# Optimization experiments

Measured on AMD Instinct MI355X. Metric: run time of the kernel, lower is better.

Reference implementation:

```python
import jax, jax.numpy as jnp
import numpy as np

B, S, H, J, LAT, OBS = 256, 128, 1024, 12, 64, 51
NL = 13                  # fk_model link count
PD = (NL + 1) * 3        # pos_dim = 42
FPS = 30.0
ACT_SCALE = 0.25
SMIN, SMAX = 0.05, 0.5
PIN = 2 * J + OBS + LAT  # 139


def setup_inputs() -> dict:
    key = jax.random.key(0)
    ks = jax.random.split(key, 16)
    rn = lambda k, shape, s=0.02: jax.random.normal(k, shape, dtype=jnp.float32) * s
    return dict(
        z=jax.random.normal(ks[0], (B, LAT), jnp.float32),
        obs_seq=jax.random.normal(ks[1], (B, S, OBS), jnp.float32),
        W1=rn(ks[2], (H, PIN)), b1=jnp.zeros((H,), jnp.float32),
        g1=jnp.ones((H,), jnp.float32), be1=jnp.zeros((H,), jnp.float32),
        W2=rn(ks[3], (H, H)), b2=jnp.zeros((H,), jnp.float32),
        g2=jnp.ones((H,), jnp.float32), be2=jnp.zeros((H,), jnp.float32),
        Wa1=rn(ks[4], (H, H)), ba1=jnp.zeros((H,), jnp.float32),
        Wa2=rn(ks[5], (J, H)), ba2=jnp.zeros((J,), jnp.float32),
        Wo=rn(ks[6], (3, H)), bo=jnp.zeros((3,), jnp.float32),
        Wv=rn(ks[7], (PD, H)), bv=jnp.full((PD,), -2.0, jnp.float32),  # torch init: zeros weight, bias=-2 (we keep small random W for non-degenerate grads)
        alpha_logits=jnp.full((J,), float(np.log(0.3)), jnp.float32),
        fk_W=rn(ks[8], (NL * 3, J), 0.1), fk_b=rn(ks[9], (NL * 3,), 0.1),  # linear FK surrogate
        pos_mean=rn(ks[10], (NL + 1, 3), 0.1),
        pos_std=1.0 + jax.random.uniform(ks[11], (NL + 1, 3), jnp.float32),
        joint_lower=jnp.full((J,), -2.0, jnp.float32),
        joint_upper=jnp.full((J,), 2.0, jnp.float32),
        default_dof_pos=rn(ks[12], (J,), 0.3),
    )


def _layernorm(x, g, b):
    m = jnp.mean(x, axis=-1, keepdims=True)
    v = jnp.var(x, axis=-1, keepdims=True)
    return (x - m) * jax.lax.rsqrt(v + 1e-5) * g + b


def reference(z, obs_seq, W1, b1, g1, be1, W2, b2, g2, be2, Wa1, ba1, Wa2, ba2,
              Wo, bo, Wv, bv, alpha_logits, fk_W, fk_b, pos_mean, pos_std,
              joint_lower, joint_upper, default_dof_pos):
    j_range = (joint_upper - joint_lower) / 2.0
    j_mean = (joint_upper + joint_lower) / 2.0
    alpha = jax.nn.sigmoid(alpha_logits)
    Bsz = z.shape[0]

    def step(carry, obs_t):
        pj, pdq = carry                                 # [B,J] each
        jn = (pj - j_mean) / j_range
        x = jnp.concatenate([jn, pdq, obs_t, z], axis=-1)   # [B,PIN]
        h = jax.nn.relu(_layernorm(x @ W1.T + b1, g1, be1))
        h = jax.nn.relu(_layernorm(h @ W2.T + b2, g2, be2))  # [B,H]
        a = jnp.tanh(jax.nn.relu(h @ Wa1.T + ba1) @ Wa2.T + ba2)  # [B,J]
        tgt = a * ACT_SCALE + default_dof_pos
        cj = jnp.clip(pj + alpha * (tgt - pj), joint_lower, joint_upper)
        obj = h @ Wo.T + bo                             # [B,3]
        # torch detaches the carried state (prev_joints/prev_dq)
        cdq = (cj - pj) * FPS
        new_carry = (jax.lax.stop_gradient(cj), jax.lax.stop_gradient(cdq))
        return new_carry, (h, a, cj, obj)

    pj0 = jnp.broadcast_to(default_dof_pos, (Bsz, J))
    pdq0 = jnp.zeros((Bsz, J), z.dtype)
    _, (hs, acts, joints, objs) = jax.lax.scan(step, (pj0, pdq0), jnp.swapaxes(obs_seq, 0, 1))

    features_seq = jnp.swapaxes(hs, 0, 1)    # [B,S,H]
    actions_seq = jnp.swapaxes(acts, 0, 1)   # [B,S,J]
    joint_traj = jnp.swapaxes(joints, 0, 1)  # [B,S,J]
    object_traj = jnp.swapaxes(objs, 0, 1)   # [B,S,3]

    agent_traj = joint_traj @ fk_W.T + fk_b  # [B,S,NL*3] linear FK surrogate
    combined = jnp.concatenate([agent_traj, object_traj], axis=-1)
    combined = combined.reshape(Bsz, S, NL + 1, 3)
    graph_x_mu = ((combined - pos_mean) / pos_std).reshape(Bsz, S, -1)  # [B,S,PD]

    sigma = SMIN + (SMAX - SMIN) * jax.nn.sigmoid(features_seq @ Wv.T + bv)
    log_sigma_pos = jnp.log(sigma)           # [B,S,PD]
    return (graph_x_mu, joint_traj, actions_seq, log_sigma_pos)
```

## Files before the change

kernel.cpp:

```cpp
#include <hip/hip_runtime.h>
#include <math.h>


#define NB 256
#define NS 128
#define NH 1024
#define NJ 12
#define NPIN 139
#define NPD 42
#define WPG 32
#define BROW 32
#define W2S 1032
#define AS 1032
#define SLOTSTRIDE 1024

typedef __attribute__((ext_vector_type(8))) short short8;
typedef __attribute__((ext_vector_type(4))) float f32x4;
typedef __attribute__((ext_vector_type(4))) unsigned short u16x4;

struct Params {
  const float* z; const float* obs; const float* W1; const float* b1;
  const float* g1; const float* be1; const float* W2; const float* b2;
  const float* g2; const float* be2; const float* Wa1; const float* ba1;
  const float* Wa2; const float* ba2; const float* Wo; const float* bo;
  const float* Wv; const float* bv; const float* alog; const float* fkW;
  const float* fkb; const float* pmean; const float* pstd; const float* jlo;
  const float* jhi; const float* ddp;
  float* out_gmu; float* out_joint; float* out_act; float* out_ls;
  float* zc; float* pa; float* part1; float* part2;
  unsigned short* y1b; unsigned short* y2b;
  unsigned short* wa1b; unsigned short* wexb;
  unsigned int* gcnt; unsigned int* slots;
};

__device__ __forceinline__ unsigned short f2bf(float x) {
  union { float f; unsigned u; } v; v.f = x;
  unsigned r = v.u + 0x7FFFu + ((v.u >> 16) & 1u);
  return (unsigned short)(r >> 16);
}
__device__ __forceinline__ float bf2f(unsigned short x) {
  union { unsigned u; float f; } v; v.u = ((unsigned)x) << 16;
  return v.f;
}
__device__ __forceinline__ unsigned cvt_pk_bf16(float lo, float hi) {
  unsigned r;
  asm("v_cvt_pk_bf16_f32 %0, %1, %2" : "=v"(r) : "v"(lo), "v"(hi));
  return r;
}
__device__ __forceinline__ void ld16_sc0(const unsigned short* p, short8& d) {
  asm volatile("global_load_dwordx4 %0, %1, off sc0" : "=v"(d) : "v"(p));
}
__device__ __forceinline__ void ldf4_sc0(const float* p, f32x4& d) {
  asm volatile("global_load_dwordx4 %0, %1, off sc0" : "=v"(d) : "v"(p));
}
__device__ __forceinline__ void vwait0() {
  asm volatile("s_waitcnt vmcnt(0)" ::: "memory");
  __builtin_amdgcn_sched_barrier(0);
}

__device__ __forceinline__ f32x4 dot1024(const unsigned short* a, const unsigned short* b) {
  const short8* ap = (const short8*)a;
  const short8* bp = (const short8*)b;
  f32x4 acc0 = {0.f, 0.f, 0.f, 0.f};
  f32x4 acc1 = {0.f, 0.f, 0.f, 0.f};
#pragma unroll 4
  for (int k8 = 0; k8 < 128; k8 += 8) {
    acc0 = __builtin_amdgcn_mfma_f32_16x16x32_bf16(ap[k8], bp[k8], acc0, 0, 0, 0);
    acc1 = __builtin_amdgcn_mfma_f32_16x16x32_bf16(ap[k8 + 4], bp[k8 + 4], acc1, 0, 0, 0);
  }
  return acc0 + acc1;
}

__device__ __forceinline__ void gbar(unsigned int* c, unsigned int target) {
  __threadfence();
  __syncthreads();
  if (threadIdx.x == 0) {
    __hip_atomic_fetch_add(c, 1u, __ATOMIC_RELEASE, __HIP_MEMORY_SCOPE_AGENT);
    unsigned long long t0 = __builtin_amdgcn_s_memrealtime();
    while (__hip_atomic_load(c, __ATOMIC_ACQUIRE, __HIP_MEMORY_SCOPE_AGENT) < target) {
      __builtin_amdgcn_s_sleep(16);
      if (__builtin_amdgcn_s_memrealtime() - t0 > (1ull << 25)) break;
    }
  }
  __syncthreads();
  __threadfence();
}

__device__ __forceinline__ void slot_wait(const unsigned int* sg, unsigned target, int lane) {
  const unsigned int* myslot = sg + (size_t)(lane & 31) * SLOTSTRIDE;
  unsigned long long t0 = __builtin_amdgcn_s_memrealtime();
  for (;;) {
    unsigned v;
    asm volatile("global_load_dword %0, %1, off sc0 sc1\n\t"
                 "s_waitcnt vmcnt(0)"
                 : "=v"(v) : "v"(myslot) : "memory");
    if (__all(v >= target)) break;
    __builtin_amdgcn_s_sleep(1);
    if (__builtin_amdgcn_s_memrealtime() - t0 > (1ull << 23)) break;
  }
}

__device__ __forceinline__ void xbar2(unsigned int* sg, int w, unsigned target,
                                      int wave, int lane) {
  asm volatile("s_waitcnt vmcnt(0)" ::: "memory");
  __syncthreads();
  if (wave == 0) {
    if (lane == 0)
      __hip_atomic_fetch_add(sg + (size_t)w * SLOTSTRIDE, 1u, __ATOMIC_RELAXED,
                             __HIP_MEMORY_SCOPE_AGENT);
    slot_wait(sg, target, lane);
  }
  __syncthreads();
}

__global__ __launch_bounds__(256, 1) void decoder_persistent(Params p) {
  __shared__ unsigned short w2l[BROW * W2S];
  __shared__ unsigned short albuf[BROW * AS];
  __shared__ float g1l[NH], be1l[NH], g2l[NH], be2l[NH];
  __shared__ unsigned short t1l[BROW * 40];
  __shared__ unsigned short wa2l[16 * 40];
  __shared__ float pj_l[BROW * NJ], pdq_l[BROW * NJ];
  __shared__ float alpha_l[NJ], jm_l[NJ], jri_l[NJ], lo_l[NJ], hi_l[NJ], ddp_l[NJ], ba2_l[NJ];
  __shared__ float pm_l[NPD], psi_l[NPD], bv_l[NPD], bo_l[4];

  const int tid = threadIdx.x;
  const int bid = blockIdx.x;
  const int g = bid & 7;
  const int w = bid >> 3;
  const int b0 = g * BROW;
  const int n0 = w * 32;
  const int wave = tid >> 6;
  const int lane = tid & 63;

  unsigned int* sg = p.slots + (size_t)g * WPG * SLOTSTRIDE;
  unsigned short* y1bg = p.y1b + (size_t)g * BROW * NH;
  unsigned short* y2bg = p.y2b + (size_t)g * BROW * NH;
  float* pa_gg = p.pa + (size_t)g * BROW * NJ * 32;
  float* part1g = p.part1 + (size_t)g * BROW * 64;
  float* part2g = p.part2 + (size_t)g * BROW * 128;

  if (tid < NJ) {
    alpha_l[tid] = 1.f / (1.f + expf(-p.alog[tid]));
    float lo = p.jlo[tid], hi = p.jhi[tid];
    jm_l[tid] = 0.5f * (hi + lo);
    jri_l[tid] = 2.f / (hi - lo);
    lo_l[tid] = lo; hi_l[tid] = hi;
    ddp_l[tid] = p.ddp[tid]; ba2_l[tid] = p.ba2[tid];
  }
  if (tid < NPD) { pm_l[tid] = p.pmean[tid]; psi_l[tid] = 1.f / p.pstd[tid]; bv_l[tid] = p.bv[tid]; }
  if (tid < 3) bo_l[tid] = p.bo[tid];
  for (int idx = tid; idx < BROW * NJ; idx += 256) { pj_l[idx] = p.ddp[idx % NJ]; pdq_l[idx] = 0.f; }
  for (int idx = tid; idx < NH; idx += 256) {
    g1l[idx] = p.g1[idx]; be1l[idx] = p.be1[idx];
    g2l[idx] = p.g2[idx]; be2l[idx] = p.be2[idx];
  }
  for (int idx = tid; idx < BROW * NH; idx += 256) {
    int r = idx >> 10, k = idx & (NH - 1);
    w2l[r * W2S + k] = f2bf(p.W2[(size_t)(n0 + r) * NH + k]);
  }
  for (int idx = tid; idx < 16 * 32; idx += 256) {
    int rr = idx >> 5, cc = idx & 31;
    wa2l[rr * 40 + cc] = (rr < NJ) ? f2bf(p.Wa2[(size_t)rr * NH + n0 + cc]) : (unsigned short)0;
  }
  {
    int r = tid >> 3, cq = tid & 7;
    int nb = n0 + cq * 4;
    const float* zr = p.z + (size_t)(b0 + r) * 64;
    const float* w1r = p.W1 + (size_t)nb * NPIN + 75;
    float a0 = p.b1[nb], a1 = p.b1[nb + 1], a2 = p.b1[nb + 2], a3 = p.b1[nb + 3];
    for (int k = 0; k < 64; ++k) {
      float zv = zr[k];
      a0 += zv * w1r[k]; a1 += zv * w1r[NPIN + k];
      a2 += zv * w1r[2 * NPIN + k]; a3 += zv * w1r[3 * NPIN + k];
    }
    f32x4 st = {a0, a1, a2, a3};
    *(f32x4*)(p.zc + (size_t)(b0 + r) * NH + nb) = st;
  }
  for (int idx = tid; idx < 4 * NH; idx += 256) {
    int r = idx >> 10, k = idx & (NH - 1);
    int row = n0 + g * 4 + r;
    p.wa1b[(size_t)row * NH + k] = f2bf(p.Wa1[(size_t)row * NH + k]);
  }
  if (bid == 1) {
    for (int idx = tid; idx < 48 * NH; idx += 256) {
      int r = idx >> 10, k = idx & (NH - 1);
      unsigned short v = 0;
      if (r < 3) v = f2bf(p.Wo[(size_t)r * NH + k]);
      else if (r < 45) v = f2bf(p.Wv[(size_t)(r - 3) * NH + k]);
      p.wexb[idx] = v;
    }
  }
  gbar(p.gcnt, 256u);

  auto stage_ln_apply = [&](const unsigned short* yg, const float* part, bool wide,
                            const float* gl, const float* bl) {
    const int r = tid >> 3, cq = tid & 7;
    const unsigned short* src = yg + (size_t)r * NH + cq * 8;
    unsigned short* dst = &albuf[r * AS + cq * 8];
    short8 v[16];
#pragma unroll
    for (int i = 0; i < 16; ++i) ld16_sc0(src + (size_t)i * 64, v[i]);
    const int fpr = wide ? 128 : 64;
    const float* pp = part + (size_t)r * fpr + cq * (fpr >> 3);
    f32x4 p0, p1, p2 = {0, 0, 0, 0}, p3 = {0, 0, 0, 0};
    ldf4_sc0(pp, p0);
    ldf4_sc0(pp + 4, p1);
    if (wide) { ldf4_sc0(pp + 8, p2); ldf4_sc0(pp + 12, p3); }
    vwait0();
    float s = p0[0] + p0[2] + p1[0] + p1[2];
    float q = p0[1] + p0[3] + p1[1] + p1[3];
    if (wide) {
      s += p2[0] + p2[2] + p3[0] + p3[2];
      q += p2[1] + p2[3] + p3[1] + p3[3];
    }
#pragma unroll
    for (int off = 4; off; off >>= 1) {
      s += __shfl_down(s, off, 8);
      q += __shfl_down(q, off, 8);
    }
    s = __shfl(s, 0, 8); q = __shfl(q, 0, 8);
    float m = s * (1.f / 1024.f);
    float rs = rsqrtf(q * (1.f / 1024.f) - m * m + 1e-5f);
    float nmrs = -m * rs;
#pragma unroll
    for (int i = 0; i < 16; ++i) {
      int c = cq * 8 + i * 64;
      f32x4 ga = *(const f32x4*)(gl + c);
      f32x4 gb = *(const f32x4*)(gl + c + 4);
      f32x4 ba = *(const f32x4*)(bl + c);
      f32x4 bb = *(const f32x4*)(bl + c + 4);
      float xn[8];
#pragma unroll
      for (int jj = 0; jj < 8; ++jj) {
        float x = bf2f((unsigned short)v[i][jj]);
        float tn = fmaf(x, rs, nmrs);
        float gg = (jj < 4) ? ga[jj] : gb[jj - 4];
        float bv2 = (jj < 4) ? ba[jj] : bb[jj - 4];
        xn[jj] = fmaxf(fmaf(tn, gg, bv2), 0.f);
      }
      uint4 pk = {cvt_pk_bf16(xn[0], xn[1]), cvt_pk_bf16(xn[2], xn[3]),
                  cvt_pk_bf16(xn[4], xn[5]), cvt_pk_bf16(xn[6], xn[7])};
      *(uint4*)(dst + i * 64) = pk;
    }
  };

  auto P1_obs = [&](int t) -> f32x4 {
    int r = tid >> 3, cq = tid & 7;
    int nb = n0 + cq * 4;
    f32x4 acc = *(const f32x4*)(p.zc + (size_t)(b0 + r) * NH + nb);
    const float* w1r = p.W1 + (size_t)nb * NPIN;
    const float* ob = p.obs + ((size_t)(b0 + r) * NS + t) * 51;
    for (int o = 0; o < 51; ++o) {
      float ov = ob[o];
      acc[0] += ov * w1r[24 + o]; acc[1] += ov * w1r[NPIN + 24 + o];
      acc[2] += ov * w1r[2 * NPIN + 24 + o]; acc[3] += ov * w1r[3 * NPIN + 24 + o];
    }
    return acc;
  };
  auto P1_fin = [&](f32x4 acc) {
    int r = tid >> 3, cq = tid & 7;
    int nb = n0 + cq * 4;
    float xj[24];
#pragma unroll
    for (int j = 0; j < NJ; ++j) {
      xj[j] = (pj_l[r * NJ + j] - jm_l[j]) * jri_l[j];
      xj[12 + j] = pdq_l[r * NJ + j];
    }
    const float* w1r = p.W1 + (size_t)nb * NPIN;
#pragma unroll
    for (int k = 0; k < 24; ++k) {
      float xv = xj[k];
      acc[0] += xv * w1r[k]; acc[1] += xv * w1r[NPIN + k];
      acc[2] += xv * w1r[2 * NPIN + k]; acc[3] += xv * w1r[3 * NPIN + k];
    }
    u16x4 hv = {f2bf(acc[0]), f2bf(acc[1]), f2bf(acc[2]), f2bf(acc[3])};
    *(u16x4*)(y1bg + (size_t)r * NH + nb) = hv;
    float s = acc[0] + acc[1] + acc[2] + acc[3];
    float q = acc[0] * acc[0] + acc[1] * acc[1] + acc[2] * acc[2] + acc[3] * acc[3];
#pragma unroll
    for (int off = 4; off; off >>= 1) {
      s += __shfl_down(s, off, 8);
      q += __shfl_down(q, off, 8);
    }
    if ((tid & 7) == 0) {
      float* pw = part1g + (size_t)r * 64 + w * 2;
      pw[0] = s; pw[1] = q;
    }
  };

  auto Yphase = [&]() {
    stage_ln_apply(y1bg, part1g, false, g1l, be1l);
    __syncthreads();
    int rt = wave >> 1, ct = wave & 1;
    int kq = (lane >> 4) * 8;
    const unsigned short* a = &albuf[(rt * 16 + (lane & 15)) * AS + kq];
    const unsigned short* b = &w2l[(ct * 16 + (lane & 15)) * W2S + kq];
    f32x4 acc = dot1024(a, b);
    int col = n0 + ct * 16 + (lane & 15);
    float b2v = p.b2[col];
    float sv[4], qv[4];
#pragma unroll
    for (int i = 0; i < 4; ++i) {
      int row = rt * 16 + (lane >> 4) * 4 + i;
      float val = acc[i] + b2v;
      y2bg[(size_t)row * NH + col] = f2bf(val);
      sv[i] = val; qv[i] = val * val;
    }
#pragma unroll
    for (int mask = 1; mask < 16; mask <<= 1) {
#pragma unroll
      for (int i = 0; i < 4; ++i) {
        sv[i] += __shfl_xor(sv[i], mask, 64);
        qv[i] += __shfl_xor(qv[i], mask, 64);
      }
    }
    if ((lane & 15) == 0) {
      int rbase = rt * 16 + (lane >> 4) * 4;
#pragma unroll
      for (int i = 0; i < 4; ++i) {
        float* pw = part2g + (size_t)(rbase + i) * 128 + (w * 2 + ct) * 2;
        pw[0] = sv[i]; pw[1] = qv[i];
      }
    }
  };

  auto Zphase = [&](int t) {
    stage_ln_apply(y2bg, part2g, true, g2l, be2l);
    __syncthreads();
    int rt = wave >> 1, ct = wave & 1;
    int kq = (lane >> 4) * 8;
    {
      const unsigned short* a = &albuf[(rt * 16 + (lane & 15)) * AS + kq];
      const unsigned short* b = p.wa1b + (size_t)(n0 + ct * 16 + (lane & 15)) * NH + kq;
      f32x4 acc = dot1024(a, b);
      int lcol = ct * 16 + (lane & 15);
      float bav = p.ba1[n0 + lcol];
#pragma unroll
      for (int i = 0; i < 4; ++i) {
        int row = rt * 16 + (lane >> 4) * 4 + i;
        t1l[row * 40 + lcol] = f2bf(fmaxf(acc[i] + bav, 0.f));
      }
    }
    __syncthreads();
    if (wave < 2) {
      int k0 = (lane >> 4) * 8;
      short8 a8 = *(const short8*)&t1l[(wave * 16 + (lane & 15)) * 40 + k0];
      short8 b8 = *(const short8*)&wa2l[(lane & 15) * 40 + k0];
      f32x4 z4 = {0.f, 0.f, 0.f, 0.f};
      f32x4 d = __builtin_amdgcn_mfma_f32_16x16x32_bf16(a8, b8, z4, 0, 0, 0);
      int j = lane & 15;
      if (j < NJ) {
#pragma unroll
        for (int i = 0; i < 4; ++i) {
          int row = wave * 16 + (lane >> 4) * 4 + i;
          pa_gg[((size_t)row * NJ + j) * 32 + w] = d[i];
        }
      }
    }
    if (w >= 26 && wave == 3) {
      int e = w - 26, cte = e >> 1, rte = e & 1;
      const unsigned short* a = &albuf[(rte * 16 + (lane & 15)) * AS + kq];
      const unsigned short* b = p.wexb + (size_t)(cte * 16 + (lane & 15)) * NH + kq;
      f32x4 acc = dot1024(a, b);
      int ec = cte * 16 + (lane & 15);
#pragma unroll
      for (int i = 0; i < 4; ++i) {
        int row = rte * 16 + (lane >> 4) * 4 + i;
        int bb = b0 + row;
        if (ec < 3) {
          float val = acc[i] + bo_l[ec];
          p.out_gmu[((size_t)bb * NS + t) * NPD + 39 + ec] = (val - pm_l[39 + ec]) * psi_l[39 + ec];
        } else if (ec < 45) {
          int sv2 = ec - 3;
          float val = acc[i] + bv_l[sv2];
          float sig = 0.05f + 0.45f / (1.f + expf(-val));
          p.out_ls[((size_t)bb * NS + t) * NPD + sv2] = logf(sig);
        }
      }
    }
  };

  auto Xmid = [&](int tp) {
    for (int e = tid; e < BROW * NJ; e += 256) {
      const float* pp = pa_gg + (size_t)e * 32;
      f32x4 u[8];
#pragma unroll
      for (int c2 = 0; c2 < 8; ++c2) ldf4_sc0(pp + c2 * 4, u[c2]);
      vwait0();
      f32x4 ss = ((u[0] + u[1]) + (u[2] + u[3])) + ((u[4] + u[5]) + (u[6] + u[7]));
      float sum = ss[0] + ss[1] + ss[2] + ss[3];
      int r = e / NJ, j = e - r * NJ;
      float av = tanhf(sum + ba2_l[j]);
      float pj = pj_l[e];
      float tgt = av * 0.25f + ddp_l[j];
      float cj = pj + alpha_l[j] * (tgt - pj);
      cj = fminf(fmaxf(cj, lo_l[j]), hi_l[j]);
      pdq_l[e] = (cj - pj) * 30.f;
      pj_l[e] = cj;
      if (w == 0) {
        size_t o = ((size_t)(b0 + r) * NS + tp) * NJ + j;
        p.out_joint[o] = cj;
        p.out_act[o] = av;
      }
    }
    __syncthreads();
    if (w == 0) {
      for (int idx = tid; idx < BROW * 39; idx += 256) {
        int r = idx / 39, m = idx - r * 39;
        float s = p.fkb[m];
        const float* fw = p.fkW + m * NJ;
#pragma unroll
        for (int j = 0; j < NJ; ++j) s += pj_l[r * NJ + j] * fw[j];
        p.out_gmu[((size_t)(b0 + r) * NS + tp) * NPD + m] = (s - pm_l[m]) * psi_l[m];
      }
    }
  };

  unsigned nbar = 0;
  {
    f32x4 acc = P1_obs(0);
    P1_fin(acc);
    xbar2(sg, w, ++nbar, wave, lane);
  }
  for (int t = 0; t < NS; ++t) {
    Yphase();
    xbar2(sg, w, ++nbar, wave, lane);
    Zphase(t);
    unsigned tc = ++nbar;
    asm volatile("s_waitcnt vmcnt(0)" ::: "memory");
    __syncthreads();
    if (tid == 0)
      __hip_atomic_fetch_add(sg + (size_t)w * SLOTSTRIDE, 1u, __ATOMIC_RELAXED,
                             __HIP_MEMORY_SCOPE_AGENT);
    f32x4 acc = {0.f, 0.f, 0.f, 0.f};
    if (t + 1 < NS) acc = P1_obs(t + 1);
    if (wave == 0) slot_wait(sg, tc, lane);
    __syncthreads();
    Xmid(t);
    if (t + 1 < NS) {
      P1_fin(acc);
      xbar2(sg, w, ++nbar, wave, lane);
    }
  }
}

extern "C" void kernel_launch(void* const* d_in, const int* in_sizes, int n_in,
                              void* d_out, int out_size, void* d_ws, size_t ws_size,
                              hipStream_t stream) {
  (void)in_sizes; (void)n_in; (void)out_size; (void)ws_size;
  char* ws = (char*)d_ws;
  Params p;
  p.z = (const float*)d_in[0];   p.obs = (const float*)d_in[1];
  p.W1 = (const float*)d_in[2];  p.b1 = (const float*)d_in[3];
  p.g1 = (const float*)d_in[4];  p.be1 = (const float*)d_in[5];
  p.W2 = (const float*)d_in[6];  p.b2 = (const float*)d_in[7];
  p.g2 = (const float*)d_in[8];  p.be2 = (const float*)d_in[9];
  p.Wa1 = (const float*)d_in[10]; p.ba1 = (const float*)d_in[11];
  p.Wa2 = (const float*)d_in[12]; p.ba2 = (const float*)d_in[13];
  p.Wo = (const float*)d_in[14]; p.bo = (const float*)d_in[15];
  p.Wv = (const float*)d_in[16]; p.bv = (const float*)d_in[17];
  p.alog = (const float*)d_in[18];
  p.fkW = (const float*)d_in[19]; p.fkb = (const float*)d_in[20];
  p.pmean = (const float*)d_in[21]; p.pstd = (const float*)d_in[22];
  p.jlo = (const float*)d_in[23]; p.jhi = (const float*)d_in[24];
  p.ddp = (const float*)d_in[25];

  float* out = (float*)d_out;
  p.out_gmu = out;
  p.out_joint = out + (size_t)256 * 128 * 42;
  p.out_act = p.out_joint + (size_t)256 * 128 * 12;
  p.out_ls = p.out_act + (size_t)256 * 128 * 12;

  p.gcnt = (unsigned int*)(ws + 0);
  p.slots = (unsigned int*)(ws + 4096);
  size_t off = 4096 + (size_t)8 * WPG * SLOTSTRIDE * 4;
  p.zc = (float*)(ws + off);                 off += (size_t)NB * NH * 4;
  p.y1b = (unsigned short*)(ws + off);       off += (size_t)NB * NH * 2;
  p.y2b = (unsigned short*)(ws + off);       off += (size_t)NB * NH * 2;
  p.pa = (float*)(ws + off);                 off += (size_t)8 * 32 * 12 * 32 * 4;
  p.part1 = (float*)(ws + off);              off += (size_t)8 * 32 * 64 * 4;
  p.part2 = (float*)(ws + off);              off += (size_t)8 * 32 * 128 * 4;
  p.wa1b = (unsigned short*)(ws + off);      off += (size_t)NH * NH * 2;
  p.wexb = (unsigned short*)(ws + off);

  hipMemsetAsync(d_ws, 0, 4096 + (size_t)8 * WPG * SLOTSTRIDE * 4, stream);
  decoder_persistent<<<dim3(256), dim3(256), 0, stream>>>(p);
}
```

Baseline: 3.669 ms.

## Remove per-step cross-block barrier by recomputing joint-input term redundantly per block

The first-layer contribution of the 24 joint/velocity inputs is now computed inside every block for the full 1024 columns with small bf16 MFMAs against a pre-converted W1 slice. The observation+latent part is precomputed one step ahead at the end of Zphase. This lets each block build its full pre-LayerNorm row locally and take LN statistics directly, dropping the partial-sum exchange and one global cross-block barrier per timestep. In exchange, each block does redundant tiny matmuls, rounds the joint term to bf16 before LN, and rereads y1b with an extra elementwise add pass.

```diff
diff --git a/kernel.cpp b/kernel.cpp
--- a/kernel.cpp
+++ b/kernel.cpp
@@ -12,6 +12,7 @@
 #define BROW 32
 #define W2S 1032
 #define AS 1032
+#define XJS 40
 #define SLOTSTRIDE 1024
 
 typedef __attribute__((ext_vector_type(8))) short short8;
@@ -27,9 +28,9 @@
   const float* fkb; const float* pmean; const float* pstd; const float* jlo;
   const float* jhi; const float* ddp;
   float* out_gmu; float* out_joint; float* out_act; float* out_ls;
-  float* zc; float* pa; float* part1; float* part2;
+  float* zc; float* pa; float* part2;
   unsigned short* y1b; unsigned short* y2b;
-  unsigned short* wa1b; unsigned short* wexb;
+  unsigned short* wa1b; unsigned short* wexb; unsigned short* w1ab;
   unsigned int* gcnt; unsigned int* slots;
 };
 
@@ -99,7 +100,6 @@
     if (__builtin_amdgcn_s_memrealtime() - t0 > (1ull << 23)) break;
   }
 }
-
 __device__ __forceinline__ void xbar2(unsigned int* sg, int w, unsigned target,
                                       int wave, int lane) {
   asm volatile("s_waitcnt vmcnt(0)" ::: "memory");
@@ -119,6 +119,7 @@
   __shared__ float g1l[NH], be1l[NH], g2l[NH], be2l[NH];
   __shared__ unsigned short t1l[BROW * 40];
   __shared__ unsigned short wa2l[16 * 40];
+  __shared__ unsigned short xjl[BROW * XJS];
   __shared__ float pj_l[BROW * NJ], pdq_l[BROW * NJ];
   __shared__ float alpha_l[NJ], jm_l[NJ], jri_l[NJ], lo_l[NJ], hi_l[NJ], ddp_l[NJ], ba2_l[NJ];
   __shared__ float pm_l[NPD], psi_l[NPD], bv_l[NPD], bo_l[4];
@@ -136,7 +137,6 @@
   unsigned short* y1bg = p.y1b + (size_t)g * BROW * NH;
   unsigned short* y2bg = p.y2b + (size_t)g * BROW * NH;
   float* pa_gg = p.pa + (size_t)g * BROW * NJ * 32;
-  float* part1g = p.part1 + (size_t)g * BROW * 64;
   float* part2g = p.part2 + (size_t)g * BROW * 128;
 
   if (tid < NJ) {
@@ -162,24 +162,47 @@
     int rr = idx >> 5, cc = idx & 31;
     wa2l[rr * 40 + cc] = (rr < NJ) ? f2bf(p.Wa2[(size_t)rr * NH + n0 + cc]) : (unsigned short)0;
   }
+  __syncthreads();
+  for (int idx = tid; idx < BROW * 32; idx += 256) {
+    int r = idx >> 5, k = idx & 31;
+    float v = 0.f;
+    if (k < NJ) v = (pj_l[r * NJ + k] - jm_l[k]) * jri_l[k];
+    else if (k < 24) v = pdq_l[r * NJ + (k - 12)];
+    xjl[r * XJS + k] = f2bf(v);
+  }
   {
     int r = tid >> 3, cq = tid & 7;
     int nb = n0 + cq * 4;
     const float* zr = p.z + (size_t)(b0 + r) * 64;
-    const float* w1r = p.W1 + (size_t)nb * NPIN + 75;
+    const float* w1z = p.W1 + (size_t)nb * NPIN + 75;
     float a0 = p.b1[nb], a1 = p.b1[nb + 1], a2 = p.b1[nb + 2], a3 = p.b1[nb + 3];
     for (int k = 0; k < 64; ++k) {
       float zv = zr[k];
-      a0 += zv * w1r[k]; a1 += zv * w1r[NPIN + k];
-      a2 += zv * w1r[2 * NPIN + k]; a3 += zv * w1r[3 * NPIN + k];
+      a0 += zv * w1z[k]; a1 += zv * w1z[NPIN + k];
+      a2 += zv * w1z[2 * NPIN + k]; a3 += zv * w1z[3 * NPIN + k];
     }
     f32x4 st = {a0, a1, a2, a3};
     *(f32x4*)(p.zc + (size_t)(b0 + r) * NH + nb) = st;
+    const float* w1r = p.W1 + (size_t)nb * NPIN;
+    const float* ob = p.obs + (size_t)(b0 + r) * NS * 51;
+    for (int o = 0; o < 51; ++o) {
+      float ov = ob[o];
+      st[0] += ov * w1r[24 + o]; st[1] += ov * w1r[NPIN + 24 + o];
+      st[2] += ov * w1r[2 * NPIN + 24 + o]; st[3] += ov * w1r[3 * NPIN + 24 + o];
+    }
+    u16x4 hv = {f2bf(st[0]), f2bf(st[1]), f2bf(st[2]), f2bf(st[3])};
+    *(u16x4*)(y1bg + (size_t)r * NH + nb) = hv;
   }
   for (int idx = tid; idx < 4 * NH; idx += 256) {
     int r = idx >> 10, k = idx & (NH - 1);
     int row = n0 + g * 4 + r;
     p.wa1b[(size_t)row * NH + k] = f2bf(p.Wa1[(size_t)row * NH + k]);
+  }
+  if (tid < 128) {
+    int c2 = tid >> 5, k = tid & 31;
+    int col = n0 + g * 4 + c2;
+    p.w1ab[(size_t)col * 32 + k] =
+        (k < 24) ? f2bf(p.W1[(size_t)col * NPIN + k]) : (unsigned short)0;
   }
   if (bid == 1) {
     for (int idx = tid; idx < 48 * NH; idx += 256) {
@@ -192,26 +215,46 @@
   }
   gbar(p.gcnt, 256u);
 
-  auto stage_ln_apply = [&](const unsigned short* yg, const float* part, bool wide,
-                            const float* gl, const float* bl) {
+  auto Ycorr = [&]() {
+    const int kq = (lane >> 4) * 8;
+    const int r0 = (lane >> 4) * 4;
+    short8 a0 = *(const short8*)&xjl[(lane & 15) * XJS + kq];
+    short8 a1 = *(const short8*)&xjl[(16 + (lane & 15)) * XJS + kq];
+#pragma unroll
+    for (int nt = 0; nt < 16; ++nt) {
+      int col = (wave * 16 + nt) * 16 + (lane & 15);
+      short8 b8 = *(const short8*)(p.w1ab + (size_t)col * 32 + kq);
+      f32x4 z4 = {0.f, 0.f, 0.f, 0.f};
+      f32x4 d0 = __builtin_amdgcn_mfma_f32_16x16x32_bf16(a0, b8, z4, 0, 0, 0);
+      f32x4 d1 = __builtin_amdgcn_mfma_f32_16x16x32_bf16(a1, b8, z4, 0, 0, 0);
+#pragma unroll
+      for (int i = 0; i < 4; ++i) {
+        albuf[(r0 + i) * AS + col] = f2bf(d0[i]);
+        albuf[(16 + r0 + i) * AS + col] = f2bf(d1[i]);
+      }
+    }
+  };
+
+  auto Ystage = [&]() {
     const int r = tid >> 3, cq = tid & 7;
-    const unsigned short* src = yg + (size_t)r * NH + cq * 8;
+    const unsigned short* src = y1bg + (size_t)r * NH + cq * 8;
     unsigned short* dst = &albuf[r * AS + cq * 8];
-    short8 v[16];
-#pragma unroll
-    for (int i = 0; i < 16; ++i) ld16_sc0(src + (size_t)i * 64, v[i]);
-    const int fpr = wide ? 128 : 64;
-    const float* pp = part + (size_t)r * fpr + cq * (fpr >> 3);
-    f32x4 p0, p1, p2 = {0, 0, 0, 0}, p3 = {0, 0, 0, 0};
-    ldf4_sc0(pp, p0);
-    ldf4_sc0(pp + 4, p1);
-    if (wide) { ldf4_sc0(pp + 8, p2); ldf4_sc0(pp + 12, p3); }
+    short8 vp[16];
+#pragma unroll
+    for (int i = 0; i < 16; ++i) ld16_sc0(src + (size_t)i * 64, vp[i]);
     vwait0();
-    float s = p0[0] + p0[2] + p1[0] + p1[2];
-    float q = p0[1] + p0[3] + p1[1] + p1[3];
-    if (wide) {
-      s += p2[0] + p2[2] + p3[0] + p3[2];
-      q += p2[1] + p2[3] + p3[1] + p3[3];
+    float s = 0.f, q = 0.f;
+#pragma unroll
+    for (int i = 0; i < 16; ++i) {
+      short8 vc = *(const short8*)(dst + i * 64);
+      short8 vs;
+#pragma unroll
+      for (int jj = 0; jj < 8; ++jj) {
+        float x = bf2f((unsigned short)vp[i][jj]) + bf2f((unsigned short)vc[jj]);
+        s += x; q = fmaf(x, x, q);
+        vs[jj] = (short)f2bf(x);
+      }
+      vp[i] = vs;
     }
 #pragma unroll
     for (int off = 4; off; off >>= 1) {
@@ -225,14 +268,14 @@
 #pragma unroll
     for (int i = 0; i < 16; ++i) {
       int c = cq * 8 + i * 64;
-      f32x4 ga = *(const f32x4*)(gl + c);
-      f32x4 gb = *(const f32x4*)(gl + c + 4);
-      f32x4 ba = *(const f32x4*)(bl + c);
-      f32x4 bb = *(const f32x4*)(bl + c + 4);
+      f32x4 ga = *(const f32x4*)(g1l + c);
+      f32x4 gb = *(const f32x4*)(g1l + c + 4);
+      f32x4 ba = *(const f32x4*)(be1l + c);
+      f32x4 bb = *(const f32x4*)(be1l + c + 4);
       float xn[8];
 #pragma unroll
       for (int jj = 0; jj < 8; ++jj) {
-        float x = bf2f((unsigned short)v[i][jj]);
+        float x = bf2f((unsigned short)vp[i][jj]);
         float tn = fmaf(x, rs, nmrs);
         float gg = (jj < 4) ? ga[jj] : gb[jj - 4];
         float bv2 = (jj < 4) ? ba[jj] : bb[jj - 4];
@@ -244,52 +287,10 @@
     }
   };
 
-  auto P1_obs = [&](int t) -> f32x4 {
-    int r = tid >> 3, cq = tid & 7;
-    int nb = n0 + cq * 4;
-    f32x4 acc = *(const f32x4*)(p.zc + (size_t)(b0 + r) * NH + nb);
-    const float* w1r = p.W1 + (size_t)nb * NPIN;
-    const float* ob = p.obs + ((size_t)(b0 + r) * NS + t) * 51;
-    for (int o = 0; o < 51; ++o) {
-      float ov = ob[o];
-      acc[0] += ov * w1r[24 + o]; acc[1] += ov * w1r[NPIN + 24 + o];
-      acc[2] += ov * w1r[2 * NPIN + 24 + o]; acc[3] += ov * w1r[3 * NPIN + 24 + o];
-    }
-    return acc;
-  };
-  auto P1_fin = [&](f32x4 acc) {
-    int r = tid >> 3, cq = tid & 7;
-    int nb = n0 + cq * 4;
-    float xj[24];
-#pragma unroll
-    for (int j = 0; j < NJ; ++j) {
-      xj[j] = (pj_l[r * NJ + j] - jm_l[j]) * jri_l[j];
-      xj[12 + j] = pdq_l[r * NJ + j];
-    }
-    const float* w1r = p.W1 + (size_t)nb * NPIN;
-#pragma unroll
-    for (int k = 0; k < 24; ++k) {
-      float xv = xj[k];
-      acc[0] += xv * w1r[k]; acc[1] += xv * w1r[NPIN + k];
-      acc[2] += xv * w1r[2 * NPIN + k]; acc[3] += xv * w1r[3 * NPIN + k];
-    }
-    u16x4 hv = {f2bf(acc[0]), f2bf(acc[1]), f2bf(acc[2]), f2bf(acc[3])};
-    *(u16x4*)(y1bg + (size_t)r * NH + nb) = hv;
-    float s = acc[0] + acc[1] + acc[2] + acc[3];
-    float q = acc[0] * acc[0] + acc[1] * acc[1] + acc[2] * acc[2] + acc[3] * acc[3];
-#pragma unroll
-    for (int off = 4; off; off >>= 1) {
-      s += __shfl_down(s, off, 8);
-      q += __shfl_down(q, off, 8);
-    }
-    if ((tid & 7) == 0) {
-      float* pw = part1g + (size_t)r * 64 + w * 2;
-      pw[0] = s; pw[1] = q;
-    }
-  };
-
   auto Yphase = [&]() {
-    stage_ln_apply(y1bg, part1g, false, g1l, be1l);
+    Ycorr();
+    __syncthreads();
+    Ystage();
     __syncthreads();
     int rt = wave >> 1, ct = wave & 1;
     int kq = (lane >> 4) * 8;
@@ -324,8 +325,53 @@
     }
   };
 
+  auto Zstage = [&]() {
+    const int r = tid >> 3, cq = tid & 7;
+    const unsigned short* src = y2bg + (size_t)r * NH + cq * 8;
+    unsigned short* dst = &albuf[r * AS + cq * 8];
+    short8 v[16];
+#pragma unroll
+    for (int i = 0; i < 16; ++i) ld16_sc0(src + (size_t)i * 64, v[i]);
+    const float* pp = part2g + (size_t)r * 128 + cq * 16;
+    f32x4 p0, p1, p2, p3;
+    ldf4_sc0(pp, p0); ldf4_sc0(pp + 4, p1);
+    ldf4_sc0(pp + 8, p2); ldf4_sc0(pp + 12, p3);
+    vwait0();
+    float s = p0[0] + p0[2] + p1[0] + p1[2] + p2[0] + p2[2] + p3[0] + p3[2];
+    float q = p0[1] + p0[3] + p1[1] + p1[3] + p2[1] + p2[3] + p3[1] + p3[3];
+#pragma unroll
+    for (int off = 4; off; off >>= 1) {
+      s += __shfl_down(s, off, 8);
+      q += __shfl_down(q, off, 8);
+    }
+    s = __shfl(s, 0, 8); q = __shfl(q, 0, 8);
+    float m = s * (1.f / 1024.f);
+    float rs = rsqrtf(q * (1.f / 1024.f) - m * m + 1e-5f);
+    float nmrs = -m * rs;
+#pragma unroll
+    for (int i = 0; i < 16; ++i) {
+      int c = cq * 8 + i * 64;
+      f32x4 ga = *(const f32x4*)(g2l + c);
+      f32x4 gb = *(const f32x4*)(g2l + c + 4);
+      f32x4 ba = *(const f32x4*)(be2l + c);
+      f32x4 bb = *(const f32x4*)(be2l + c + 4);
+      float xn[8];
+#pragma unroll
+      for (int jj = 0; jj < 8; ++jj) {
+        float x = bf2f((unsigned short)v[i][jj]);
+        float tn = fmaf(x, rs, nmrs);
+        float gg = (jj < 4) ? ga[jj] : gb[jj - 4];
+        float bv2 = (jj < 4) ? ba[jj] : bb[jj - 4];
+        xn[jj] = fmaxf(fmaf(tn, gg, bv2), 0.f);
+      }
+      uint4 pk = {cvt_pk_bf16(xn[0], xn[1]), cvt_pk_bf16(xn[2], xn[3]),
+                  cvt_pk_bf16(xn[4], xn[5]), cvt_pk_bf16(xn[6], xn[7])};
+      *(uint4*)(dst + i * 64) = pk;
+    }
+  };
+
   auto Zphase = [&](int t) {
-    stage_ln_apply(y2bg, part2g, true, g2l, be2l);
+    Zstage();
     __syncthreads();
     int rt = wave >> 1, ct = wave & 1;
     int kq = (lane >> 4) * 8;
@@ -377,6 +423,20 @@
           p.out_ls[((size_t)bb * NS + t) * NPD + sv2] = logf(sig);
         }
       }
+    }
+    if (t + 1 < NS) {
+      int r = tid >> 3, cq = tid & 7;
+      int nb = n0 + cq * 4;
+      f32x4 acc = *(const f32x4*)(p.zc + (size_t)(b0 + r) * NH + nb);
+      const float* w1r = p.W1 + (size_t)nb * NPIN;
+      const float* ob = p.obs + ((size_t)(b0 + r) * NS + (t + 1)) * 51;
+      for (int o = 0; o < 51; ++o) {
+        float ov = ob[o];
+        acc[0] += ov * w1r[24 + o]; acc[1] += ov * w1r[NPIN + 24 + o];
+        acc[2] += ov * w1r[2 * NPIN + 24 + o]; acc[3] += ov * w1r[3 * NPIN + 24 + o];
+      }
+      u16x4 hv = {f2bf(acc[0]), f2bf(acc[1]), f2bf(acc[2]), f2bf(acc[3])};
+      *(u16x4*)(y1bg + (size_t)r * NH + nb) = hv;
     }
   };
 
@@ -414,33 +474,23 @@
         p.out_gmu[((size_t)(b0 + r) * NS + tp) * NPD + m] = (s - pm_l[m]) * psi_l[m];
       }
     }
+    for (int idx = tid; idx < BROW * 32; idx += 256) {
+      int r = idx >> 5, k = idx & 31;
+      float v = 0.f;
+      if (k < NJ) v = (pj_l[r * NJ + k] - jm_l[k]) * jri_l[k];
+      else if (k < 24) v = pdq_l[r * NJ + (k - 12)];
+      xjl[r * XJS + k] = f2bf(v);
+    }
+    __syncthreads();
   };
 
   unsigned nbar = 0;
-  {
-    f32x4 acc = P1_obs(0);
-    P1_fin(acc);
-    xbar2(sg, w, ++nbar, wave, lane);
-  }
   for (int t = 0; t < NS; ++t) {
     Yphase();
     xbar2(sg, w, ++nbar, wave, lane);
     Zphase(t);
-    unsigned tc = ++nbar;
-    asm volatile("s_waitcnt vmcnt(0)" ::: "memory");
-    __syncthreads();
-    if (tid == 0)
-      __hip_atomic_fetch_add(sg + (size_t)w * SLOTSTRIDE, 1u, __ATOMIC_RELAXED,
-                             __HIP_MEMORY_SCOPE_AGENT);
-    f32x4 acc = {0.f, 0.f, 0.f, 0.f};
-    if (t + 1 < NS) acc = P1_obs(t + 1);
-    if (wave == 0) slot_wait(sg, tc, lane);
-    __syncthreads();
+    xbar2(sg, w, ++nbar, wave, lane);
     Xmid(t);
-    if (t + 1 < NS) {
-      P1_fin(acc);
-      xbar2(sg, w, ++nbar, wave, lane);
-    }
   }
 }
 
@@ -478,10 +528,10 @@
   p.y1b = (unsigned short*)(ws + off);       off += (size_t)NB * NH * 2;
   p.y2b = (unsigned short*)(ws + off);       off += (size_t)NB * NH * 2;
   p.pa = (float*)(ws + off);                 off += (size_t)8 * 32 * 12 * 32 * 4;
-  p.part1 = (float*)(ws + off);              off += (size_t)8 * 32 * 64 * 4;
   p.part2 = (float*)(ws + off);              off += (size_t)8 * 32 * 128 * 4;
   p.wa1b = (unsigned short*)(ws + off);      off += (size_t)NH * NH * 2;
-  p.wexb = (unsigned short*)(ws + off);
+  p.wexb = (unsigned short*)(ws + off);      off += (size_t)48 * NH * 2;
+  p.w1ab = (unsigned short*)(ws + off);      off += (size_t)NH * 32 * 2;
 
   hipMemsetAsync(d_ws, 0, 4096 + (size_t)8 * WPG * SLOTSTRIDE * 4, stream);
   decoder_persistent<<<dim3(256), dim3(256), 0, stream>>>(p);
```

New measurement: 3.718 ms. No clear change (+1.3%).
